# Kernel tuning notes

Measured on AMD Instinct MI355X. Metric: run time of the kernel, lower is better.

The kernel has to match this reference:

```python
import jax, jax.numpy as jnp
import numpy as np

NUM_CLASSES = 4
LAMBDA_CREDA = 1.0
LAMBDA_ENTROPY = 0.1
SIGMA = 32.0          # config.sigma (fixed, not 'auto')
USE_UNCERTAINTY = True
EPS = 1e-8
LOG2 = float(np.log(2.0))

N_S, N_T, D = 4096, 4096, 1024


def _rbf(x, y, sigma):
    # squared euclidean distances (== torch.cdist(x,y)**2), then gaussian kernel
    d2 = (jnp.sum(x * x, axis=1)[:, None] + jnp.sum(y * y, axis=1)[None, :]
          - 2.0 * (x @ y.T))
    d2 = jnp.maximum(d2, 0.0)
    return jnp.exp(-d2 / (2.0 * sigma * sigma + EPS))


def _h2(tr, sumsq):
    # H2(A) = -log2(tr(A@A)), A = K/(tr(K)+eps); tr(A@A) = sum(K*K)/(tr+eps)^2 for symmetric K
    info = sumsq / (tr + EPS) ** 2
    return -jnp.log(info + EPS) / LOG2


def setup_inputs() -> dict:
    key = jax.random.key(0)
    k1, k2, k3, k4, k5 = jax.random.split(key, 5)
    return {
        "features_s": jax.random.normal(k1, (N_S, D), dtype=jnp.float32),
        "logits_s": jax.random.normal(k2, (N_S, NUM_CLASSES), dtype=jnp.float32),
        "features_t": jax.random.normal(k3, (N_T, D), dtype=jnp.float32),
        "logits_t": jax.random.normal(k4, (N_T, NUM_CLASSES), dtype=jnp.float32),
        "labels_s": jax.random.randint(k5, (N_S,), 0, NUM_CLASSES, dtype=jnp.int32),
    }


def reference(features_s, logits_s, features_t, logits_t, labels_s):
    # ---- classification loss (cross entropy on source) ----
    logp_s = jax.nn.log_softmax(logits_s, axis=1)
    loss_cls = -jnp.mean(jnp.take_along_axis(logp_s, labels_s[:, None], axis=1))

    # ---- target entropy loss ----
    probs_t = jax.nn.softmax(logits_t, axis=1)
    loss_ent = -jnp.mean(jnp.sum(probs_t * jnp.log(probs_t + EPS), axis=1))

    # ---- pseudo labels + uncertainty weights ----
    pseudo_t = jnp.argmax(jax.lax.stop_gradient(probs_t), axis=1)
    if USE_UNCERTAINTY:
        h2_probs = -jnp.log(jnp.sum(probs_t ** 2, axis=1) + EPS) / LOG2
        h2_max = np.log(float(NUM_CLASSES)) / LOG2
        w = 1.0 - h2_probs / (h2_max + EPS)          # [N_t]
    else:
        w = jnp.ones((features_t.shape[0],), dtype=probs_t.dtype)

    # ---- shared RBF kernel blocks (sigma fixed -> identical across classes) ----
    K_ss = _rbf(features_s, features_s, SIGMA)       # [N_s, N_s]
    K_tt = _rbf(features_t, features_t, SIGMA)       # [N_t, N_t]
    K_st = _rbf(features_s, features_t, SIGMA)       # [N_s, N_t]

    # per-class masks (zero-masking a kernel preserves trace and trace(K@K))
    Ms = jax.nn.one_hot(labels_s, NUM_CLASSES, dtype=K_ss.dtype).T   # [C, N_s]
    Mt = jax.nn.one_hot(pseudo_t, NUM_CLASSES, dtype=K_tt.dtype).T   # [C, N_t]
    Wt = Mt * w[None, :]                                             # [C, N_t]
    Wt2 = Wt * Wt

    n_s = jnp.sum(Ms, axis=1)                        # class counts (source)
    n_t = jnp.sum(Mt, axis=1)                        # class counts (target)

    # traces: diag(K)=1, target block weighted by outer(w,w)
    tr_s = n_s                                       # [C]
    tr_t = jnp.sum(Wt2, axis=1)                      # [C]

    # sum of squared entries of the masked (and weighted) blocks
    ss_s = jnp.einsum('ci,ci->c', Ms @ (K_ss ** 2), Ms)     # tr(K_s^2) per class
    ss_t = jnp.einsum('ci,ci->c', Wt2 @ (K_tt ** 2), Wt2)   # tr(K_tw^2) per class
    ss_st = jnp.einsum('ci,ci->c', Ms @ (K_st ** 2), Mt)    # sum(K_st^2) per class

    h_s = _h2(tr_s, ss_s)
    h_t = _h2(tr_t, ss_t)
    h_mix = _h2(tr_s + tr_t, ss_s + 2.0 * ss_st + ss_t)

    per_class = h_mix - 0.5 * (h_s + h_t)            # [C]
    valid = (n_s >= 2) & (n_t >= 2)
    n_valid = jnp.sum(valid.astype(per_class.dtype))
    creda_sum = jnp.sum(jnp.where(valid, per_class, 0.0))
    loss_creda = jnp.where(n_valid > 0, creda_sum / jnp.maximum(n_valid, 1.0), 0.0)

    total_loss = loss_cls + LAMBDA_CREDA * loss_creda + LAMBDA_ENTROPY * loss_ent
    return total_loss
```

## Files before the change

kernel.cpp:

```cpp
#include <hip/hip_runtime.h>
#include <cstdint>
#include <cstddef>

#define NS_ROWS 4096
#define NT_ROWS 4096
#define DIM 1024
#define NC 4
#define NWORK_MAX 2432
#define ACC_N 26

typedef __attribute__((ext_vector_type(4))) float f32x4;
typedef long long i64;

#define GLOBAL_AS __attribute__((address_space(1)))
#define LDS_AS __attribute__((address_space(3)))


__device__ __forceinline__ int argmax4(float4 l) {
    int am = 0; float bm = l.x;
    if (l.y > bm) { bm = l.y; am = 1; }
    if (l.z > bm) { bm = l.z; am = 2; }
    if (l.w > bm) { bm = l.w; am = 3; }
    return am;
}

__global__ __launch_bounds__(1024)
void rank_prep(const int* __restrict__ labels, const float* __restrict__ LS,
               const float* __restrict__ LT,
               int* __restrict__ ctrl, float* __restrict__ acc,
               int* __restrict__ dstS, int* __restrict__ dstT) {
    __shared__ unsigned long long wtot[16];
    __shared__ float wred[16];
    __shared__ float cls4[NC];
    int t = threadIdx.x;
    int wid = t >> 6, lane = t & 63;
    bool isS = (blockIdx.x == 0);
    int* dst = isS ? dstS : dstT;
    const float EPSF = 1e-8f;
    const float INV_LOG2 = 1.44269504088896340736f;

    if (t < NC) cls4[t] = 0.f;

    int c4[4];
    float localScalar = 0.f;
    float localW2[NC] = {0.f, 0.f, 0.f, 0.f};
    if (isS) {
        int4 lab4 = ((const int4*)labels)[t];
        c4[0] = lab4.x; c4[1] = lab4.y; c4[2] = lab4.z; c4[3] = lab4.w;
#pragma unroll
        for (int i = 0; i < 4; ++i) {
            float4 l = ((const float4*)LS)[t * 4 + i];
            float m = fmaxf(fmaxf(l.x, l.y), fmaxf(l.z, l.w));
            float e = expf(l.x - m) + expf(l.y - m) + expf(l.z - m) + expf(l.w - m);
            float lse = m + logf(e);
            int lab = c4[i];
            float ll = (lab == 0) ? l.x : (lab == 1) ? l.y : (lab == 2) ? l.z : l.w;
            localScalar += lse - ll;
        }
    } else {
#pragma unroll
        for (int i = 0; i < 4; ++i) {
            float4 l = ((const float4*)LT)[t * 4 + i];
            int am = argmax4(l);
            c4[i] = am;
            float m = fmaxf(fmaxf(l.x, l.y), fmaxf(l.z, l.w));
            float p0 = expf(l.x - m), p1 = expf(l.y - m),
                  p2 = expf(l.z - m), p3 = expf(l.w - m);
            float s = p0 + p1 + p2 + p3;
            p0 /= s; p1 /= s; p2 /= s; p3 /= s;
            localScalar += p0 * logf(p0 + EPSF) + p1 * logf(p1 + EPSF) +
                           p2 * logf(p2 + EPSF) + p3 * logf(p3 + EPSF);
            float sumsq = p0 * p0 + p1 * p1 + p2 * p2 + p3 * p3;
            float h2 = -logf(sumsq + EPSF) * INV_LOG2;
            float w = 1.0f - h2 / (2.0f + EPSF);
            localW2[am] += w * w;
        }
    }

    unsigned long long packed = 0ULL;
#pragma unroll
    for (int i = 0; i < 4; ++i) packed += 1ULL << (c4[i] * 16);
    unsigned long long v = packed;
#pragma unroll
    for (int off = 1; off < 64; off <<= 1) {
        unsigned long long n = __shfl_up(v, off);
        if (lane >= off) v += n;
    }
    if (lane == 63) wtot[wid] = v;
    __syncthreads();
    if (t < 16) {
        unsigned long long x = wtot[t];
#pragma unroll
        for (int off = 1; off < 16; off <<= 1) {
            unsigned long long n = __shfl_up(x, off);
            if (lane >= off) x += n;
        }
        wtot[t] = x;
    }
    __syncthreads();
    unsigned long long incl = v + (wid > 0 ? wtot[wid - 1] : 0ULL);
    unsigned long long tot = wtot[15];
    unsigned long long ex = incl - packed;

    int baseC[NC]; int b = 0;
#pragma unroll
    for (int c = 0; c < NC; ++c) {
        baseC[c] = b;
        b += (int)((tot >> (c * 16)) & 0xFFFFULL);
    }
    if (t == 0) {
#pragma unroll
        for (int c = 0; c < NC; ++c) {
            ctrl[(isS ? 0 : 4) + c] = (int)((tot >> (c * 16)) & 0xFFFFULL);
            ctrl[(isS ? 16 : 20) + c] = baseC[c];
        }
    }
    int pref[NC];
#pragma unroll
    for (int c = 0; c < NC; ++c)
        pref[c] = (int)((ex >> (c * 16)) & 0xFFFFULL) + baseC[c];
#pragma unroll
    for (int i = 0; i < 4; ++i) {
        int c = c4[i];
        dst[t * 4 + i] = pref[c]++;
    }

    for (int off = 32; off; off >>= 1) localScalar += __shfl_xor(localScalar, off);
    if (lane == 0) wred[wid] = localScalar;
    if (!isS) {
#pragma unroll
        for (int c = 0; c < NC; ++c) {
            float x = localW2[c];
            for (int off = 32; off; off >>= 1) x += __shfl_xor(x, off);
            if (lane == 0 && x != 0.f) atomicAdd(&cls4[c], x);
        }
    }
    __syncthreads();
    if (t == 0) {
        float s = 0.f;
        for (int i = 0; i < 16; ++i) s += wred[i];
        acc[isS ? 0 : 1] = s;
    }
    if (!isS && t < NC) acc[10 + t] = cls4[t];
}

__global__ void aux_build(const int* __restrict__ ctrl, int4* __restrict__ wl,
                          int* __restrict__ ctrl_w, float* __restrict__ acc) {
    int t = threadIdx.x;
    if (t >= 12 && t < 24) acc[14 + (t - 12)] = 0.f;
    int Ts[NC], Tt[NC];
#pragma unroll
    for (int c = 0; c < NC; ++c) {
        Ts[c] = (ctrl[c] + 127) >> 7;
        Tt[c] = (ctrl[4 + c] + 127) >> 7;
    }
    int segSize[12];
#pragma unroll
    for (int c = 0; c < NC; ++c) {
        segSize[c * 3 + 0] = Ts[c] * (Ts[c] + 1) / 2;
        segSize[c * 3 + 1] = Tt[c] * (Tt[c] + 1) / 2;
        segSize[c * 3 + 2] = Ts[c] * Tt[c];
    }
    if (t == 0) {
        int n = 0;
        for (int s = 0; s < 12; ++s) n += segSize[s];
        ctrl_w[24] = n;
    }
    if (t >= 12) return;
    int base = 0;
    for (int s = 0; s < t; ++s) base += segSize[s];
    int c = t / 3, kind = t % 3;
    int4* w = wl + base;
    int n = 0;
    if (kind == 0) {
        for (int tj = 0; tj < Ts[c]; ++tj)
            for (int ti = 0; ti <= tj; ++ti) w[n++] = make_int4(0, c, ti, tj);
    } else if (kind == 1) {
        for (int tj = 0; tj < Tt[c]; ++tj)
            for (int ti = 0; ti <= tj; ++ti) w[n++] = make_int4(1, c, ti, tj);
    } else {
        for (int ti = 0; ti < Ts[c]; ++ti)
            for (int tj = 0; tj < Tt[c]; ++tj) w[n++] = make_int4(2, c, ti, tj);
    }
}

__global__ void scatter_feat(const float* __restrict__ FS, const float* __restrict__ FT,
                             const int* __restrict__ labels, const float* __restrict__ LT,
                             const int* __restrict__ dstS, const int* __restrict__ dstT,
                             unsigned char* __restrict__ fs, unsigned char* __restrict__ ft,
                             float* __restrict__ nS, float* __restrict__ wS, int* __restrict__ cS,
                             float* __restrict__ nT, float* __restrict__ wT, int* __restrict__ cT) {
    int row = blockIdx.x * 4 + (threadIdx.x >> 6);
    int lane = threadIdx.x & 63;
    bool isS = row < NS_ROWS;
    int r = isS ? row : row - NS_ROWS;
    int dst = isS ? dstS[r] : dstT[r];

    const float* src = (isS ? FS : FT) + (size_t)r * DIM;
    float4 v0 = ((const float4*)src)[lane * 4 + 0];
    float4 v1 = ((const float4*)src)[lane * 4 + 1];
    float4 v2 = ((const float4*)src)[lane * 4 + 2];
    float4 v3 = ((const float4*)src)[lane * 4 + 3];
    int w0 = 0, w1 = 0, w2 = 0, w3 = 0;
    w0 = __builtin_amdgcn_cvt_pk_fp8_f32(v0.x, v0.y, w0, false);
    w0 = __builtin_amdgcn_cvt_pk_fp8_f32(v0.z, v0.w, w0, true);
    w1 = __builtin_amdgcn_cvt_pk_fp8_f32(v1.x, v1.y, w1, false);
    w1 = __builtin_amdgcn_cvt_pk_fp8_f32(v1.z, v1.w, w1, true);
    w2 = __builtin_amdgcn_cvt_pk_fp8_f32(v2.x, v2.y, w2, false);
    w2 = __builtin_amdgcn_cvt_pk_fp8_f32(v2.z, v2.w, w2, true);
    w3 = __builtin_amdgcn_cvt_pk_fp8_f32(v3.x, v3.y, w3, false);
    w3 = __builtin_amdgcn_cvt_pk_fp8_f32(v3.z, v3.w, w3, true);

    float ssum = 0.f;
#define ACCQ(wv)                                                       \
    do {                                                               \
        float q0 = __builtin_amdgcn_cvt_f32_fp8((wv), 0);              \
        float q1 = __builtin_amdgcn_cvt_f32_fp8((wv), 1);              \
        float q2 = __builtin_amdgcn_cvt_f32_fp8((wv), 2);              \
        float q3 = __builtin_amdgcn_cvt_f32_fp8((wv), 3);              \
        ssum += q0 * q0 + q1 * q1 + q2 * q2 + q3 * q3;                 \
    } while (0)
    ACCQ(w0); ACCQ(w1); ACCQ(w2); ACCQ(w3);
#undef ACCQ

    unsigned char* fdst = (isS ? fs : ft) + (size_t)dst * DIM;
    *(uint4*)(fdst + lane * 16) = make_uint4((unsigned)w0, (unsigned)w1,
                                             (unsigned)w2, (unsigned)w3);

    for (int off = 32; off; off >>= 1) ssum += __shfl_xor(ssum, off);

    if (lane == 0) {
        if (isS) {
            nS[dst] = ssum; wS[dst] = 1.0f; cS[dst] = labels[r];
        } else {
            float4 l = ((const float4*)LT)[r];
            int am = argmax4(l);
            float m = fmaxf(fmaxf(l.x, l.y), fmaxf(l.z, l.w));
            float p0 = expf(l.x - m), p1 = expf(l.y - m),
                  p2 = expf(l.z - m), p3 = expf(l.w - m);
            float s = p0 + p1 + p2 + p3;
            float sumsq = (p0 * p0 + p1 * p1 + p2 * p2 + p3 * p3) / (s * s);
            const float INV_LOG2 = 1.44269504088896340736f;
            float h2 = -logf(sumsq + 1e-8f) * INV_LOG2;
            float w = 1.0f - h2 / (2.0f + 1e-8f);
            nT[dst] = ssum; wT[dst] = w * w; cT[dst] = am;
        }
    }
}

__global__ __launch_bounds__(256, 4)
void gemm_reduce(const unsigned char* __restrict__ fs, const unsigned char* __restrict__ ft,
                 const float* __restrict__ nS, const float* __restrict__ wS, const int* __restrict__ cS,
                 const float* __restrict__ nT, const float* __restrict__ wT, const int* __restrict__ cT,
                 const int* __restrict__ ctrl, const int4* __restrict__ wl,
                 float* __restrict__ acc) {
    __shared__ unsigned char As[2][128 * 64];
    __shared__ unsigned char Bs[2][128 * 64];
    __shared__ float sred;

    int nwork = ctrl[24];
    int chunk = (nwork + 7) >> 3;
    int sub = blockIdx.x >> 3, xcd = blockIdx.x & 7;
    if (sub >= chunk) return;
    int widx = xcd * chunk + sub;
    if (widx >= nwork) return;
    int4 it = wl[widx];
    int kind = it.x, cls = it.y, ti = it.z, tj = it.w;

    const unsigned char *A, *B;
    const float *nA, *nB, *wA, *wB;
    const int *cA, *cB;
    int baseA, baseB;
    if (kind == 0)      { A = fs; B = fs; nA = nS; nB = nS; wA = wS; wB = wS; cA = cS; cB = cS;
                          baseA = ctrl[16 + cls]; baseB = baseA; }
    else if (kind == 1) { A = ft; B = ft; nA = nT; nB = nT; wA = wT; wB = wT; cA = cT; cB = cT;
                          baseA = ctrl[20 + cls]; baseB = baseA; }
    else                { A = fs; B = ft; nA = nS; nB = nT; wA = wS; cA = cS; cB = cT;
                          wB = wS;
                          baseA = ctrl[16 + cls]; baseB = ctrl[20 + cls]; }
    float* outp = acc + 14 + kind * 4 + cls;
    float factor = (kind != 2 && ti != tj) ? 2.0f : 1.0f;

    int tid = threadIdx.x;
    int lane = tid & 63;
    int wid = tid >> 6;
    int wr = wid >> 1, wc = wid & 1;

    int rowA0 = baseA + ti * 128;
    int rowB0 = baseB + tj * 128;

    int srow = tid >> 2;
    int sb = (((tid & 3) ^ ((tid >> 3) & 3))) * 16;

    const unsigned char* pa0 = A + (size_t)min(rowA0 + srow,      4095) * DIM + sb;
    const unsigned char* pa1 = A + (size_t)min(rowA0 + srow + 64, 4095) * DIM + sb;
    const unsigned char* pb0 = B + (size_t)min(rowB0 + srow,      4095) * DIM + sb;
    const unsigned char* pb1 = B + (size_t)min(rowB0 + srow + 64, 4095) * DIM + sb;

    f32x4 accf[4][4];
#pragma unroll
    for (int m = 0; m < 4; ++m)
#pragma unroll
        for (int n = 0; n < 4; ++n) accf[m][n] = (f32x4)(0.f);

    int lr = lane & 15;
    int lk = (lane >> 4) * 8;
    int sw = (lr >> 1) & 3;

#define STAGE(buf, kt)                                                            \
    do {                                                                          \
        int k0_ = (kt) * 64;                                                      \
        __builtin_amdgcn_global_load_lds((const GLOBAL_AS void*)(pa0 + k0_),      \
            (LDS_AS void*)(As[buf] + tid * 16), 16, 0, 0);                        \
        __builtin_amdgcn_global_load_lds((const GLOBAL_AS void*)(pa1 + k0_),      \
            (LDS_AS void*)(As[buf] + 4096 + tid * 16), 16, 0, 0);                 \
        __builtin_amdgcn_global_load_lds((const GLOBAL_AS void*)(pb0 + k0_),      \
            (LDS_AS void*)(Bs[buf] + tid * 16), 16, 0, 0);                        \
        __builtin_amdgcn_global_load_lds((const GLOBAL_AS void*)(pb1 + k0_),      \
            (LDS_AS void*)(Bs[buf] + 4096 + tid * 16), 16, 0, 0);                 \
    } while (0)

#define COMPUTE_HALF(buf, kk)                                                     \
    do {                                                                          \
        int b_ = (kk) + lk;                                                       \
        int bs_ = ((((b_) >> 4) ^ sw) << 4) | ((b_) & 15);     \
        i64 af[4], bfr[4];                                                        \
        _Pragma("unroll")                                                         \
        for (int f = 0; f < 4; ++f)                                               \
            af[f] = *(const i64*)(As[buf] + (wr * 64 + f * 16 + lr) * 64 + bs_);  \
        _Pragma("unroll")                                                         \
        for (int f = 0; f < 4; ++f)                                               \
            bfr[f] = *(const i64*)(Bs[buf] + (wc * 64 + f * 16 + lr) * 64 + bs_); \
        _Pragma("unroll")                                                         \
        for (int m = 0; m < 4; ++m)                                               \
            _Pragma("unroll")                                                     \
            for (int n = 0; n < 4; ++n)                                           \
                accf[m][n] = __builtin_amdgcn_mfma_f32_16x16x32_fp8_fp8(          \
                    af[m], bfr[n], accf[m][n], 0, 0, 0);                          \
    } while (0)

    STAGE(0, 0);
    asm volatile("s_waitcnt vmcnt(0)");
    __syncthreads();

    int cur = 0;
    for (int kt = 0; kt < DIM / 64 - 1; ++kt) {
        STAGE(cur ^ 1, kt + 1);
        COMPUTE_HALF(cur, 0);
        COMPUTE_HALF(cur, 32);
        __syncthreads();
        cur ^= 1;
    }
    COMPUTE_HALF(cur, 0);
    COMPUTE_HALF(cur, 32);

    int rowBase = rowA0 + wr * 64;
    int colBase = rowB0 + wc * 64;

    float cn[4], cw[4];
#pragma unroll
    for (int f = 0; f < 4; ++f) {
        int gj = colBase + f * 16 + lr;
        int gjc = min(gj, 4095);
        cn[f] = nB[gjc];
        cw[f] = (gj < 4096 && cB[gjc] == cls) ? wB[gjc] : 0.0f;
    }

    const float NEGF = (-2.0f / (2.0f * 32.0f * 32.0f + 1e-8f)) * 1.44269504088896340736f;
    float lacc = 0.f;

#pragma unroll
    for (int m = 0; m < 4; ++m) {
#pragma unroll
        for (int j = 0; j < 4; ++j) {
            int gi = rowBase + m * 16 + (lane >> 4) * 4 + j;
            int gic = min(gi, 4095);
            float rn = nA[gic];
            float rw = (gi < 4096 && cA[gic] == cls) ? wA[gic] : 0.0f;
#pragma unroll
            for (int n = 0; n < 4; ++n) {
                float dot = accf[m][n][j];
                float d2 = rn + cn[n] - 2.0f * dot;
                d2 = fmaxf(d2, 0.0f);
                float k2 = exp2f(d2 * NEGF);
                lacc += k2 * rw * cw[n];
            }
        }
    }

    if (tid == 0) sred = 0.f;
    __syncthreads();
    for (int off = 32; off; off >>= 1) lacc += __shfl_xor(lacc, off);
    if (lane == 0) atomicAdd(&sred, lacc);
    __syncthreads();
    if (tid == 0) atomicAdd(outp, factor * sred);
#undef STAGE
#undef COMPUTE_HALF
}

__global__ void finalize_kernel(const float* __restrict__ acc, const int* __restrict__ ctrl,
                                float* __restrict__ out) {
    if (threadIdx.x != 0 || blockIdx.x != 0) return;
    const double EPS = 1e-8;
    const double LOG2 = 0.6931471805599453;
    double loss_cls = (double)acc[0] / NS_ROWS;
    double loss_ent = -(double)acc[1] / NT_ROWS;
    double creda_sum = 0.0, n_valid = 0.0;
    for (int c = 0; c < NC; ++c) {
        int nsc_i = ctrl[c], ntc_i = ctrl[4 + c];
        double nsc = (double)nsc_i, trt = acc[10 + c];
        double sss = acc[14 + c], sst = acc[18 + c], ssst = acc[22 + c];
        double trs = nsc;
        double info_s = sss / ((trs + EPS) * (trs + EPS));
        double h_s = -log(info_s + EPS) / LOG2;
        double info_t = sst / ((trt + EPS) * (trt + EPS));
        double h_t = -log(info_t + EPS) / LOG2;
        double trm = trs + trt;
        double ssm = sss + 2.0 * ssst + sst;
        double info_m = ssm / ((trm + EPS) * (trm + EPS));
        double h_m = -log(info_m + EPS) / LOG2;
        double pc = h_m - 0.5 * (h_s + h_t);
        if (nsc_i >= 2 && ntc_i >= 2) { creda_sum += pc; n_valid += 1.0; }
    }
    double creda = (n_valid > 0.0) ? creda_sum / n_valid : 0.0;
    out[0] = (float)(loss_cls + 1.0 * creda + 0.1 * loss_ent);
}

extern "C" void kernel_launch(void* const* d_in, const int* in_sizes, int n_in,
                              void* d_out, int out_size, void* d_ws, size_t ws_size,
                              hipStream_t stream) {
    const float* FS = (const float*)d_in[0];
    const float* LS = (const float*)d_in[1];
    const float* FT = (const float*)d_in[2];
    const float* LT = (const float*)d_in[3];
    const int* LAB = (const int*)d_in[4];

    char* ws = (char*)d_ws;
    unsigned char* fs = (unsigned char*)(ws);
    unsigned char* ft = (unsigned char*)(ws + 4194304);
    char* p = ws + 8388608;
    float* nS  = (float*)(p);
    float* wS  = (float*)(p + 16384);
    int*   cS  = (int*)  (p + 32768);
    float* nT  = (float*)(p + 49152);
    float* wT  = (float*)(p + 65536);
    int*   cT  = (int*)  (p + 81920);
    int*   ctrl = (int*)  (p + 98304);
    float* acc  = (float*)(p + 98304 + 128);
    int4*  wl   = (int4*) (p + 98304 + 512);
    int*   dstS = (int*)  (p + 98304 + 512 + NWORK_MAX * 16);
    int*   dstT = dstS + NS_ROWS;

    rank_prep<<<2, 1024, 0, stream>>>(LAB, LS, LT, ctrl, acc, dstS, dstT);
    aux_build<<<1, 64, 0, stream>>>(ctrl, wl, ctrl, acc);
    scatter_feat<<<2048, 256, 0, stream>>>(FS, FT, LAB, LT, dstS, dstT, fs, ft,
                                           nS, wS, cS, nT, wT, cT);
    gemm_reduce<<<NWORK_MAX, 256, 0, stream>>>(fs, ft, nS, wS, cS, nT, wT, cT,
                                               ctrl, wl, acc);
    finalize_kernel<<<1, 1, 0, stream>>>(acc, ctrl, (float*)d_out);
}
```

Baseline: 65.15 us.

## Triple-buffer GEMM loads, fuse aux build into scatter, finalize in last block

The work-list build is merged into the scatter kernel as an extra block, and the finalize step moves into the last finishing GEMM block through an atomic counter. This removes two kernel launches and their gaps. The GEMM main loop goes from double to triple buffering with partial vmcnt waits, so loads run two stages ahead. That costs 50% more LDS and lowers the occupancy hint from 4 to 3. The last-block finalize relies on threadfence and atomic ordering, and the counter is reset inside the scatter kernel, which only works if every early-exiting GEMM block is accounted for.

```diff
diff --git a/kernel.cpp b/kernel.cpp
--- a/kernel.cpp
+++ b/kernel.cpp
@@ -144,52 +144,55 @@
     if (!isS && t < NC) acc[10 + t] = cls4[t];
 }
 
-__global__ void aux_build(const int* __restrict__ ctrl, int4* __restrict__ wl,
-                          int* __restrict__ ctrl_w, float* __restrict__ acc) {
-    int t = threadIdx.x;
-    if (t >= 12 && t < 24) acc[14 + (t - 12)] = 0.f;
-    int Ts[NC], Tt[NC];
-#pragma unroll
-    for (int c = 0; c < NC; ++c) {
-        Ts[c] = (ctrl[c] + 127) >> 7;
-        Tt[c] = (ctrl[4 + c] + 127) >> 7;
-    }
-    int segSize[12];
-#pragma unroll
-    for (int c = 0; c < NC; ++c) {
-        segSize[c * 3 + 0] = Ts[c] * (Ts[c] + 1) / 2;
-        segSize[c * 3 + 1] = Tt[c] * (Tt[c] + 1) / 2;
-        segSize[c * 3 + 2] = Ts[c] * Tt[c];
-    }
-    if (t == 0) {
+__global__ void scatter_aux(const float* __restrict__ FS, const float* __restrict__ FT,
+                            const int* __restrict__ labels, const float* __restrict__ LT,
+                            const int* __restrict__ dstS, const int* __restrict__ dstT,
+                            unsigned char* __restrict__ fs, unsigned char* __restrict__ ft,
+                            float* __restrict__ nS, float* __restrict__ wS, int* __restrict__ cS,
+                            float* __restrict__ nT, float* __restrict__ wT, int* __restrict__ cT,
+                            int* __restrict__ ctrl, int4* __restrict__ wl,
+                            float* __restrict__ acc) {
+    if (blockIdx.x == 2048) {
+        int t = threadIdx.x;
+        if (t >= 12 && t < 24) acc[14 + (t - 12)] = 0.f;
+        if (t == 30) ctrl[25] = 0;
+        int Ts[NC], Tt[NC];
+#pragma unroll
+        for (int c = 0; c < NC; ++c) {
+            Ts[c] = (ctrl[c] + 127) >> 7;
+            Tt[c] = (ctrl[4 + c] + 127) >> 7;
+        }
+        int segSize[12];
+#pragma unroll
+        for (int c = 0; c < NC; ++c) {
+            segSize[c * 3 + 0] = Ts[c] * (Ts[c] + 1) / 2;
+            segSize[c * 3 + 1] = Tt[c] * (Tt[c] + 1) / 2;
+            segSize[c * 3 + 2] = Ts[c] * Tt[c];
+        }
+        if (t == 31) {
+            int n = 0;
+            for (int s = 0; s < 12; ++s) n += segSize[s];
+            ctrl[24] = n;
+        }
+        if (t >= 12) return;
+        int base = 0;
+        for (int s = 0; s < t; ++s) base += segSize[s];
+        int c = t / 3, kind = t % 3;
+        int4* w = wl + base;
         int n = 0;
-        for (int s = 0; s < 12; ++s) n += segSize[s];
-        ctrl_w[24] = n;
-    }
-    if (t >= 12) return;
-    int base = 0;
-    for (int s = 0; s < t; ++s) base += segSize[s];
-    int c = t / 3, kind = t % 3;
-    int4* w = wl + base;
-    int n = 0;
-    if (kind == 0) {
-        for (int tj = 0; tj < Ts[c]; ++tj)
-            for (int ti = 0; ti <= tj; ++ti) w[n++] = make_int4(0, c, ti, tj);
-    } else if (kind == 1) {
-        for (int tj = 0; tj < Tt[c]; ++tj)
-            for (int ti = 0; ti <= tj; ++ti) w[n++] = make_int4(1, c, ti, tj);
-    } else {
-        for (int ti = 0; ti < Ts[c]; ++ti)
-            for (int tj = 0; tj < Tt[c]; ++tj) w[n++] = make_int4(2, c, ti, tj);
-    }
-}
-
-__global__ void scatter_feat(const float* __restrict__ FS, const float* __restrict__ FT,
-                             const int* __restrict__ labels, const float* __restrict__ LT,
-                             const int* __restrict__ dstS, const int* __restrict__ dstT,
-                             unsigned char* __restrict__ fs, unsigned char* __restrict__ ft,
-                             float* __restrict__ nS, float* __restrict__ wS, int* __restrict__ cS,
-                             float* __restrict__ nT, float* __restrict__ wT, int* __restrict__ cT) {
+        if (kind == 0) {
+            for (int tj = 0; tj < Ts[c]; ++tj)
+                for (int ti = 0; ti <= tj; ++ti) w[n++] = make_int4(0, c, ti, tj);
+        } else if (kind == 1) {
+            for (int tj = 0; tj < Tt[c]; ++tj)
+                for (int ti = 0; ti <= tj; ++ti) w[n++] = make_int4(1, c, ti, tj);
+        } else {
+            for (int ti = 0; ti < Ts[c]; ++ti)
+                for (int tj = 0; tj < Tt[c]; ++tj) w[n++] = make_int4(2, c, ti, tj);
+        }
+        return;
+    }
+
     int row = blockIdx.x * 4 + (threadIdx.x >> 6);
     int lane = threadIdx.x & 63;
     bool isS = row < NS_ROWS;
@@ -248,14 +251,14 @@
     }
 }
 
-__global__ __launch_bounds__(256, 4)
+__global__ __launch_bounds__(256, 3)
 void gemm_reduce(const unsigned char* __restrict__ fs, const unsigned char* __restrict__ ft,
                  const float* __restrict__ nS, const float* __restrict__ wS, const int* __restrict__ cS,
                  const float* __restrict__ nT, const float* __restrict__ wT, const int* __restrict__ cT,
-                 const int* __restrict__ ctrl, const int4* __restrict__ wl,
-                 float* __restrict__ acc) {
-    __shared__ unsigned char As[2][128 * 64];
-    __shared__ unsigned char Bs[2][128 * 64];
+                 int* __restrict__ ctrl, const int4* __restrict__ wl,
+                 float* __restrict__ acc, float* __restrict__ out) {
+    __shared__ unsigned char As[3][128 * 64];
+    __shared__ unsigned char Bs[3][128 * 64];
     __shared__ float sred;
 
     int nwork = ctrl[24];
@@ -323,7 +326,7 @@
 #define COMPUTE_HALF(buf, kk)                                                     \
     do {                                                                          \
         int b_ = (kk) + lk;                                                       \
-        int bs_ = ((((b_) >> 4) ^ sw) << 4) | ((b_) & 15);     \
+        int bs_ = ((((b_) >> 4) ^ sw) << 4) | ((b_) & 15);                        \
         i64 af[4], bfr[4];                                                        \
         _Pragma("unroll")                                                         \
         for (int f = 0; f < 4; ++f)                                               \
@@ -340,19 +343,27 @@
     } while (0)
 
     STAGE(0, 0);
-    asm volatile("s_waitcnt vmcnt(0)");
-    __syncthreads();
-
-    int cur = 0;
-    for (int kt = 0; kt < DIM / 64 - 1; ++kt) {
-        STAGE(cur ^ 1, kt + 1);
-        COMPUTE_HALF(cur, 0);
-        COMPUTE_HALF(cur, 32);
-        __syncthreads();
-        cur ^= 1;
-    }
-    COMPUTE_HALF(cur, 0);
-    COMPUTE_HALF(cur, 32);
+    STAGE(1, 1);
+
+    int bcur = 0;
+    for (int kt = 0; kt < DIM / 64 - 2; ++kt) {
+        asm volatile("s_waitcnt vmcnt(4)" ::: "memory");
+        __builtin_amdgcn_s_barrier();
+        int bst = bcur + 2; if (bst >= 3) bst -= 3;
+        STAGE(bst, kt + 2);
+        COMPUTE_HALF(bcur, 0);
+        COMPUTE_HALF(bcur, 32);
+        ++bcur; if (bcur == 3) bcur = 0;
+    }
+    asm volatile("s_waitcnt vmcnt(4)" ::: "memory");
+    __builtin_amdgcn_s_barrier();
+    COMPUTE_HALF(bcur, 0);
+    COMPUTE_HALF(bcur, 32);
+    ++bcur; if (bcur == 3) bcur = 0;
+    asm volatile("s_waitcnt vmcnt(0)" ::: "memory");
+    __builtin_amdgcn_s_barrier();
+    COMPUTE_HALF(bcur, 0);
+    COMPUTE_HALF(bcur, 32);
 
     int rowBase = rowA0 + wr * 64;
     int colBase = rowB0 + wc * 64;
@@ -393,37 +404,43 @@
     for (int off = 32; off; off >>= 1) lacc += __shfl_xor(lacc, off);
     if (lane == 0) atomicAdd(&sred, lacc);
     __syncthreads();
-    if (tid == 0) atomicAdd(outp, factor * sred);
+
+    if (tid == 0) {
+        atomicAdd(outp, factor * sred);
+        __threadfence();
+        int done = atomicAdd(&ctrl[25], 1);
+        if (done == nwork - 1) {
+            __threadfence();
+            const double EPS = 1e-8;
+            const double LOG2 = 0.6931471805599453;
+            double av[12];
+            for (int i = 0; i < 12; ++i)
+                av[i] = (double)atomicAdd(&acc[14 + i], 0.0f);
+            double loss_cls = (double)acc[0] / NS_ROWS;
+            double loss_ent = -(double)acc[1] / NT_ROWS;
+            double creda_sum = 0.0, n_valid = 0.0;
+            for (int c = 0; c < NC; ++c) {
+                int nsc_i = ctrl[c], ntc_i = ctrl[4 + c];
+                double trt = acc[10 + c];
+                double sss = av[c], sst = av[4 + c], ssst = av[8 + c];
+                double trs = (double)nsc_i;
+                double info_s = sss / ((trs + EPS) * (trs + EPS));
+                double h_s = -log(info_s + EPS) / LOG2;
+                double info_t = sst / ((trt + EPS) * (trt + EPS));
+                double h_t = -log(info_t + EPS) / LOG2;
+                double trm = trs + trt;
+                double ssm = sss + 2.0 * ssst + sst;
+                double info_m = ssm / ((trm + EPS) * (trm + EPS));
+                double h_m = -log(info_m + EPS) / LOG2;
+                double pc = h_m - 0.5 * (h_s + h_t);
+                if (nsc_i >= 2 && ntc_i >= 2) { creda_sum += pc; n_valid += 1.0; }
+            }
+            double creda = (n_valid > 0.0) ? creda_sum / n_valid : 0.0;
+            out[0] = (float)(loss_cls + 1.0 * creda + 0.1 * loss_ent);
+        }
+    }
 #undef STAGE
 #undef COMPUTE_HALF
-}
-
-__global__ void finalize_kernel(const float* __restrict__ acc, const int* __restrict__ ctrl,
-                                float* __restrict__ out) {
-    if (threadIdx.x != 0 || blockIdx.x != 0) return;
-    const double EPS = 1e-8;
-    const double LOG2 = 0.6931471805599453;
-    double loss_cls = (double)acc[0] / NS_ROWS;
-    double loss_ent = -(double)acc[1] / NT_ROWS;
-    double creda_sum = 0.0, n_valid = 0.0;
-    for (int c = 0; c < NC; ++c) {
-        int nsc_i = ctrl[c], ntc_i = ctrl[4 + c];
-        double nsc = (double)nsc_i, trt = acc[10 + c];
-        double sss = acc[14 + c], sst = acc[18 + c], ssst = acc[22 + c];
-        double trs = nsc;
-        double info_s = sss / ((trs + EPS) * (trs + EPS));
-        double h_s = -log(info_s + EPS) / LOG2;
-        double info_t = sst / ((trt + EPS) * (trt + EPS));
-        double h_t = -log(info_t + EPS) / LOG2;
-        double trm = trs + trt;
-        double ssm = sss + 2.0 * ssst + sst;
-        double info_m = ssm / ((trm + EPS) * (trm + EPS));
-        double h_m = -log(info_m + EPS) / LOG2;
-        double pc = h_m - 0.5 * (h_s + h_t);
-        if (nsc_i >= 2 && ntc_i >= 2) { creda_sum += pc; n_valid += 1.0; }
-    }
-    double creda = (n_valid > 0.0) ? creda_sum / n_valid : 0.0;
-    out[0] = (float)(loss_cls + 1.0 * creda + 0.1 * loss_ent);
 }
 
 extern "C" void kernel_launch(void* const* d_in, const int* in_sizes, int n_in,
@@ -452,10 +469,8 @@
     int*   dstT = dstS + NS_ROWS;
 
     rank_prep<<<2, 1024, 0, stream>>>(LAB, LS, LT, ctrl, acc, dstS, dstT);
-    aux_build<<<1, 64, 0, stream>>>(ctrl, wl, ctrl, acc);
-    scatter_feat<<<2048, 256, 0, stream>>>(FS, FT, LAB, LT, dstS, dstT, fs, ft,
-                                           nS, wS, cS, nT, wT, cT);
+    scatter_aux<<<2049, 256, 0, stream>>>(FS, FT, LAB, LT, dstS, dstT, fs, ft,
+                                          nS, wS, cS, nT, wT, cT, ctrl, wl, acc);
     gemm_reduce<<<NWORK_MAX, 256, 0, stream>>>(fs, ft, nS, wS, cS, nT, wT, cT,
-                                               ctrl, wl, acc);
-    finalize_kernel<<<1, 1, 0, stream>>>(acc, ctrl, (float*)d_out);
+                                               ctrl, wl, acc, (float*)d_out);
 }
```

Measured after the change: 69.60 us. 6.8% more time.
